# Kernel tuning notes

Hardware: AMD Instinct MI355X
Metric: run time of the kernel (lower is better)

Reference implementation:

```python
import jax, jax.numpy as jnp
import numpy as np

B, S, H = 2, 2048, 1024
E, K = 16, 2
CF = 1.5
IMP_THRESH = 0.5
CAP_MAX = int(B * S * CF * K / E)  # 768, capacity when adaptive_k == K


def setup_inputs() -> dict:
    key = jax.random.key(0)
    ks = jax.random.split(key, 8)
    def xavier(k, shape):
        fan_in, fan_out = shape[0], shape[1]
        std = np.sqrt(2.0 / (fan_in + fan_out))
        return jax.random.normal(k, shape, dtype=jnp.float32) * std
    return {
        'hidden_states': jax.random.normal(ks[0], (B, S, H), dtype=jnp.float32),
        # router: Linear(H,H) -> ReLU -> Linear(H,E)
        'W1': xavier(ks[1], (H, H)), 'b1': jnp.zeros((H,), jnp.float32),
        'W2': xavier(ks[2], (H, E)), 'b2': jnp.zeros((E,), jnp.float32),
        # importance predictor: Linear(H,H//2) -> ReLU -> Linear(H//2,1) -> Sigmoid
        'Wi1': xavier(ks[3], (H, H // 2)), 'bi1': jnp.zeros((H // 2,), jnp.float32),
        'Wi2': xavier(ks[4], (H // 2, 1)), 'bi2': jnp.zeros((1,), jnp.float32),
        # top_k predictor: Linear(H+1,H//4) -> ReLU -> Linear(H//4,K) -> Softmax
        'Wt1': xavier(ks[5], (H + 1, H // 4)), 'bt1': jnp.zeros((H // 4,), jnp.float32),
        'Wt2': xavier(ks[6], (H // 4, K)), 'bt2': jnp.zeros((K,), jnp.float32),
    }


def reference(hidden_states, W1, b1, W2, b2, Wi1, bi1, Wi2, bi2, Wt1, bt1, Wt2, bt2):
    # importance scores [B,S]
    imp_h = jax.nn.relu(hidden_states @ Wi1 + bi1)
    importance = jax.nn.sigmoid(jnp.squeeze(imp_h @ Wi2 + bi2, -1))

    # adaptive top-k (traced scalar in [1, K])
    avg_feat = hidden_states.mean((0, 1))                       # [H]
    combined = jnp.concatenate([avg_feat, importance.mean()[None]])  # [H+1]
    tk_probs = jax.nn.softmax(jax.nn.relu(combined @ Wt1 + bt1) @ Wt2 + bt2)
    adaptive_k = jnp.minimum(jnp.argmax(tk_probs) + 1, K).astype(jnp.int32)

    # router logits -> probs -> top-k
    logits = jax.nn.relu(hidden_states @ W1 + b1) @ W2 + b2     # [B,S,E]
    router_probs = jax.nn.softmax(logits, axis=-1)
    topk_p, topk_i = jax.lax.top_k(router_probs, K)             # [B,S,K], sorted desc

    # only the first adaptive_k slots are active (== torch.topk with k=adaptive_k)
    slot_valid = (jnp.arange(K) < adaptive_k)                   # [K] bool
    p = topk_p * slot_valid.astype(topk_p.dtype)
    p = p / (p.sum(-1, keepdims=True) + 1e-8)

    # capacity-limited dispatch/combine (vectorized version of the b,s,k loop)
    cap_eff = jnp.floor(jnp.float32(B * S) * CF * adaptive_k.astype(jnp.float32) / E).astype(jnp.int32)
    N = B * S * K
    e_flat = topk_i.reshape(N)                                  # expert id per (b,s,k) in loop order
    p_flat = p.reshape(N)
    valid = jnp.broadcast_to(slot_valid, (B * S, K)).reshape(N)
    oh = jax.nn.one_hot(e_flat, E, dtype=jnp.float32) * valid[:, None].astype(jnp.float32)  # [N,E]
    # position within expert = running count of earlier valid assignments to same expert
    pos = (jnp.cumsum(oh, axis=0)[jnp.arange(N), e_flat] - 1.0).astype(jnp.int32)
    write = valid & (pos >= 0) & (pos < cap_eff)
    pos_c = jnp.clip(pos, 0, CAP_MAX - 1)
    t_idx = jnp.arange(N) // K                                  # flat token index
    wf = write.astype(p_flat.dtype)
    dispatch = jnp.zeros((B * S, E, CAP_MAX), p.dtype).at[t_idx, e_flat, pos_c].add(wf)
    combine = jnp.zeros((B * S, E, CAP_MAX), p.dtype).at[t_idx, e_flat, pos_c].add(wf * p_flat)
    dispatch = dispatch.reshape(B, S, E, CAP_MAX)
    combine = combine.reshape(B, S, E, CAP_MAX)

    # load-balancing aux loss
    prob_per_expert = router_probs.mean((0, 1))                 # [E]
    usage = oh.sum(0) / (jnp.float32(B * S) * adaptive_k.astype(jnp.float32))
    aux_loss = jnp.sum(prob_per_expert * usage) * E

    # importance re-weighting of combine tensor
    iw = (importance > IMP_THRESH).astype(combine.dtype)
    combine = combine * (1.0 + iw[:, :, None, None])

    return dispatch, combine, router_probs, aux_loss, importance
```

## Files before the change

kernel.cpp:

```cpp
#include <hip/hip_runtime.h>
#include <math.h>

#define TOK   4096
#define HD    1024
#define NEXP  16
#define CAPM  768

static const size_t DISP_OFF = 0;
static const size_t COMB_OFF = 50331648;
static const size_t RP_OFF   = 100663296;
static const size_t AUX_OFF  = 100728832;
static const size_t IMP_OFF  = 100728833;

#define WS_IMPZ   0
#define WS_COLSUM 4096
#define WS_T1PRE  5120
#define WS_PROBS  5376
#define WS_AK     5392
#define WS_TOPKP  5400
#define WS_TOPKI  13592
#define WS_ZEROF  5400

typedef float v4f __attribute__((ext_vector_type(4)));

__global__ __launch_bounds__(256) void kZero(v4f* __restrict__ p, int n4)
{
    const v4f z = (v4f)(0.f);
    const int stride = gridDim.x * 256;
    for (int i = blockIdx.x * 256 + threadIdx.x; i < n4; i += stride)
        __builtin_nontemporal_store(z, p + i);
}

#define KA_ROW(i, AX) \
    acc[i][0] = fmaf(AX, f0.x, acc[i][0]); \
    acc[i][1] = fmaf(AX, f0.y, acc[i][1]); \
    acc[i][2] = fmaf(AX, f0.z, acc[i][2]); \
    acc[i][3] = fmaf(AX, f0.w, acc[i][3]); \
    acc[i][4] = fmaf(AX, f1.x, acc[i][4]); \
    acc[i][5] = fmaf(AX, f1.y, acc[i][5]); \
    acc[i][6] = fmaf(AX, f1.z, acc[i][6]); \
    acc[i][7] = fmaf(AX, f1.w, acc[i][7]);

__global__ __launch_bounds__(256, 4) void kA(
    const float* __restrict__ x, const float* __restrict__ W1,
    const float* __restrict__ b1, const float* __restrict__ Wi1,
    const float* __restrict__ bi1, const float* __restrict__ Wi2,
    float* __restrict__ h1out, float* __restrict__ impz)
{
    __shared__ __align__(16) float As[2][16][68];
    __shared__ __align__(16) float Bs[2][16][128];
    __shared__ float red[64];

    const int tid = threadIdx.x;
    const int tx = tid & 15;
    const int ty = tid >> 4;
    const int n0 = blockIdx.x * 128;
    const int m0 = blockIdx.y * 64;
    const bool isW1 = (n0 < HD);
    const float* __restrict__ Bp = isW1 ? (W1 + n0) : (Wi1 + (n0 - HD));
    const int ldb = isW1 ? 1024 : 512;

    const int am  = tid >> 2;
    const int akq = tid & 3;
    const int br = tid >> 5;
    const int bq = tid & 31;

    if (tid < 64) red[tid] = 0.f;

    float acc[4][8];
#pragma unroll
    for (int i = 0; i < 4; ++i)
#pragma unroll
        for (int j = 0; j < 8; ++j) acc[i][j] = 0.f;

    const float* pA = x + (size_t)(m0 + am) * HD + akq * 4;
    const float* pB = Bp + (size_t)br * ldb + bq * 4;

    float4 ra  = *(const float4*)(pA);
    float4 rb0 = *(const float4*)(pB);
    float4 rb1 = *(const float4*)(pB + (size_t)8 * ldb);
    {
        As[0][akq * 4 + 0][am] = ra.x;
        As[0][akq * 4 + 1][am] = ra.y;
        As[0][akq * 4 + 2][am] = ra.z;
        As[0][akq * 4 + 3][am] = ra.w;
        *(float4*)&Bs[0][br][bq * 4]     = rb0;
        *(float4*)&Bs[0][br + 8][bq * 4] = rb1;
    }
    __syncthreads();

#pragma unroll 1
    for (int kt = 0; kt < 64; ++kt) {
        const int buf = kt & 1;
        if (kt < 63) {
            const int ko = (kt + 1) * 16;
            ra  = *(const float4*)(pA + ko);
            rb0 = *(const float4*)(pB + (size_t)(ko + 0) * ldb);
            rb1 = *(const float4*)(pB + (size_t)(ko + 8) * ldb);
        }
#pragma unroll 8
        for (int kk = 0; kk < 16; ++kk) {
            const float4 a  = *(const float4*)&As[buf][kk][ty * 4];
            const float4 f0 = *(const float4*)&Bs[buf][kk][tx * 4];
            const float4 f1 = *(const float4*)&Bs[buf][kk][tx * 4 + 64];
            KA_ROW(0, a.x)
            KA_ROW(1, a.y)
            KA_ROW(2, a.z)
            KA_ROW(3, a.w)
        }
        if (kt < 63) {
            const int nb = buf ^ 1;
            As[nb][akq * 4 + 0][am] = ra.x;
            As[nb][akq * 4 + 1][am] = ra.y;
            As[nb][akq * 4 + 2][am] = ra.z;
            As[nb][akq * 4 + 3][am] = ra.w;
            *(float4*)&Bs[nb][br][bq * 4]     = rb0;
            *(float4*)&Bs[nb][br + 8][bq * 4] = rb1;
            __syncthreads();
        }
    }

    if (isW1) {
        const float4 bb0 = *(const float4*)(b1 + n0 + tx * 4);
        const float4 bb1 = *(const float4*)(b1 + n0 + tx * 4 + 64);
        const float bvv[8] = { bb0.x, bb0.y, bb0.z, bb0.w, bb1.x, bb1.y, bb1.z, bb1.w };
#pragma unroll
        for (int i = 0; i < 4; ++i) {
            const int m = m0 + ty * 4 + i;
            float4 o0, o1;
            o0.x = fmaxf(acc[i][0] + bvv[0], 0.f);
            o0.y = fmaxf(acc[i][1] + bvv[1], 0.f);
            o0.z = fmaxf(acc[i][2] + bvv[2], 0.f);
            o0.w = fmaxf(acc[i][3] + bvv[3], 0.f);
            o1.x = fmaxf(acc[i][4] + bvv[4], 0.f);
            o1.y = fmaxf(acc[i][5] + bvv[5], 0.f);
            o1.z = fmaxf(acc[i][6] + bvv[6], 0.f);
            o1.w = fmaxf(acc[i][7] + bvv[7], 0.f);
            *(float4*)(h1out + (size_t)m * HD + n0 + tx * 4)      = o0;
            *(float4*)(h1out + (size_t)m * HD + n0 + tx * 4 + 64) = o1;
        }
    } else {
        const int nW = n0 - HD;
        const float4 bb0 = *(const float4*)(bi1 + nW + tx * 4);
        const float4 bb1 = *(const float4*)(bi1 + nW + tx * 4 + 64);
        const float4 w0  = *(const float4*)(Wi2 + nW + tx * 4);
        const float4 w1  = *(const float4*)(Wi2 + nW + tx * 4 + 64);
        const float bvv[8] = { bb0.x, bb0.y, bb0.z, bb0.w, bb1.x, bb1.y, bb1.z, bb1.w };
        const float wvv[8] = { w0.x, w0.y, w0.z, w0.w, w1.x, w1.y, w1.z, w1.w };
        __syncthreads();
#pragma unroll
        for (int i = 0; i < 4; ++i) {
            float s = 0.f;
#pragma unroll
            for (int j = 0; j < 8; ++j)
                s += fmaxf(acc[i][j] + bvv[j], 0.f) * wvv[j];
            atomicAdd(&red[ty * 4 + i], s);
        }
        __syncthreads();
        if (tid < 64) atomicAdd(&impz[m0 + tid], red[tid]);
    }
}

__global__ void kSig(const float* __restrict__ impz, const float* __restrict__ bi2,
                     float* __restrict__ impOut)
{
    const int t = blockIdx.x * 256 + threadIdx.x;
    const float z = impz[t] + bi2[0];
    impOut[t] = 1.f / (1.f + expf(-z));
}

__global__ void kAvg(const float* __restrict__ x, float* __restrict__ colsum)
{
    const int c = blockIdx.x * 256 + threadIdx.x;
    const int r0 = blockIdx.y * 64;
    float s = 0.f;
    for (int r = r0; r < r0 + 64; ++r) s += x[(size_t)r * HD + c];
    atomicAdd(&colsum[c], s);
}

__global__ void kTk1(const float* __restrict__ colsum, const float* __restrict__ Wt1,
                     float* __restrict__ t1pre)
{
    const int j = threadIdx.x;
    const int i0 = blockIdx.x * 32;
    float s = 0.f;
    for (int i = i0; i < i0 + 32; ++i)
        s = fmaf(colsum[i] * (1.f / TOK), Wt1[i * 256 + j], s);
    atomicAdd(&t1pre[j], s);
}

__global__ void kTk2(const float* __restrict__ imp, const float* __restrict__ t1pre,
                     const float* __restrict__ Wt1, const float* __restrict__ bt1,
                     const float* __restrict__ Wt2, const float* __restrict__ bt2,
                     int* __restrict__ akOut)
{
    __shared__ float sm[256];
    const int tid = threadIdx.x;
    float s = 0.f;
    for (int i = 0; i < 16; ++i) s += imp[tid + i * 256];
    sm[tid] = s;
    __syncthreads();
    for (int off = 128; off > 0; off >>= 1) {
        if (tid < off) sm[tid] += sm[tid + off];
        __syncthreads();
    }
    const float imp_mean = sm[0] * (1.f / TOK);
    __syncthreads();
    const float t1 = fmaxf(t1pre[tid] + imp_mean * Wt1[1024 * 256 + tid] + bt1[tid], 0.f);
    sm[tid] = t1 * Wt2[tid * 2 + 0];
    __syncthreads();
    for (int off = 128; off > 0; off >>= 1) {
        if (tid < off) sm[tid] += sm[tid + off];
        __syncthreads();
    }
    const float l0 = sm[0] + bt2[0];
    __syncthreads();
    sm[tid] = t1 * Wt2[tid * 2 + 1];
    __syncthreads();
    for (int off = 128; off > 0; off >>= 1) {
        if (tid < off) sm[tid] += sm[tid + off];
        __syncthreads();
    }
    const float l1 = sm[0] + bt2[1];
    if (tid == 0) akOut[0] = (l1 > l0) ? 2 : 1;
}

__global__ __launch_bounds__(256) void kLog(
    const float* __restrict__ h1, const float* __restrict__ W2,
    const float* __restrict__ b2, float* __restrict__ rp,
    float* __restrict__ topkP, int* __restrict__ topkI,
    float* __restrict__ probsum)
{
    __shared__ float lg[16][17];
    __shared__ float ex[16][17];
    __shared__ float ps[16];
    const int tid = threadIdx.x;
    const int e  = tid & 15;
    const int tt = tid >> 4;
    const int t  = blockIdx.x * 16 + tt;
    const float* __restrict__ hrow = h1 + (size_t)t * HD;
    float s0 = 0.f, s1 = 0.f, s2 = 0.f, s3 = 0.f;
#pragma unroll 4
    for (int k = 0; k < HD; k += 4) {
        const float4 h = *(const float4*)(hrow + k);
        s0 = fmaf(h.x, W2[(k + 0) * NEXP + e], s0);
        s1 = fmaf(h.y, W2[(k + 1) * NEXP + e], s1);
        s2 = fmaf(h.z, W2[(k + 2) * NEXP + e], s2);
        s3 = fmaf(h.w, W2[(k + 3) * NEXP + e], s3);
    }
    const float logit = (s0 + s1) + (s2 + s3) + b2[e];
    lg[tt][e] = logit;
    if (tid < 16) ps[tid] = 0.f;
    __syncthreads();
    float mx = -1e30f;
#pragma unroll
    for (int j = 0; j < 16; ++j) mx = fmaxf(mx, lg[tt][j]);
    const float my_ex = expf(logit - mx);
    ex[tt][e] = my_ex;
    __syncthreads();
    float sum = 0.f;
#pragma unroll
    for (int j = 0; j < 16; ++j) sum += ex[tt][j];
    const float p = my_ex / sum;
    rp[(size_t)t * NEXP + e] = p;
    lg[tt][e] = p;
    atomicAdd(&ps[e], p);
    __syncthreads();
    if (e == 0) {
        float pv[16];
#pragma unroll
        for (int j = 0; j < 16; ++j) pv[j] = lg[tt][j];
        int i0 = 0; float v0 = pv[0];
#pragma unroll
        for (int j = 1; j < 16; ++j) if (pv[j] > v0) { v0 = pv[j]; i0 = j; }
        int i1 = -1; float v1 = -1e30f;
#pragma unroll
        for (int j = 0; j < 16; ++j) if (j != i0 && pv[j] > v1) { v1 = pv[j]; i1 = j; }
        topkP[t * 2] = v0; topkP[t * 2 + 1] = v1;
        topkI[t * 2] = i0; topkI[t * 2 + 1] = i1;
    }
    if (tid < 16) atomicAdd(&probsum[tid], ps[tid]);
}

__global__ __launch_bounds__(256) void kScan(
    const float* __restrict__ topkP, const int* __restrict__ topkI,
    const int* __restrict__ akPtr, const float* __restrict__ probsum,
    const float* __restrict__ imp, float* __restrict__ disp,
    float* __restrict__ comb, float* __restrict__ aux)
{
    __shared__ int cnt[256][16];
    __shared__ int totals[16];
    const int tid = threadIdx.x;
    const int ak = akPtr[0];
    const int cap = 384 * ak;
    int c[16];
#pragma unroll
    for (int e = 0; e < 16; ++e) c[e] = 0;
    const int n0 = tid * 32;
    for (int j = 0; j < 32; ++j) {
        const int n = n0 + j;
        if ((n & 1) < ak) c[topkI[n]]++;
    }
#pragma unroll
    for (int e = 0; e < 16; ++e) cnt[tid][e] = c[e];
    __syncthreads();
    if (tid < 16) {
        int run = 0;
        for (int i = 0; i < 256; ++i) { const int v = cnt[i][tid]; cnt[i][tid] = run; run += v; }
        totals[tid] = run;
    }
    __syncthreads();
#pragma unroll
    for (int e = 0; e < 16; ++e) c[e] = cnt[tid][e];
    for (int j = 0; j < 32; ++j) {
        const int n = n0 + j;
        const int k = n & 1;
        if (k < ak) {
            const int e = topkI[n];
            const int pos = c[e]++;
            if (pos < cap) {
                const int t = n >> 1;
                const float p0 = topkP[t * 2], p1 = topkP[t * 2 + 1];
                const float ssum = (ak == 2) ? (p0 + p1) : p0;
                const float pv = ((k == 0) ? p0 : p1) / (ssum + 1e-8f);
                const float iw = (imp[t] > 0.5f) ? 2.f : 1.f;
                const size_t idx = (size_t)t * (NEXP * CAPM) + (size_t)e * CAPM + pos;
                disp[idx] = 1.f;
                comb[idx] = pv * iw;
            }
        }
    }
    if (tid == 0) {
        float a = 0.f;
        const float invAk = 1.f / (float)(TOK * ak);
        for (int e = 0; e < 16; ++e)
            a += (probsum[e] * (1.f / TOK)) * ((float)totals[e] * invAk);
        aux[0] = a * (float)NEXP;
    }
}

extern "C" void kernel_launch(void* const* d_in, const int* in_sizes, int n_in,
                              void* d_out, int out_size, void* d_ws, size_t ws_size,
                              hipStream_t stream)
{
    const float* x   = (const float*)d_in[0];
    const float* W1  = (const float*)d_in[1];
    const float* b1  = (const float*)d_in[2];
    const float* W2  = (const float*)d_in[3];
    const float* b2  = (const float*)d_in[4];
    const float* Wi1 = (const float*)d_in[5];
    const float* bi1 = (const float*)d_in[6];
    const float* Wi2 = (const float*)d_in[7];
    const float* bi2 = (const float*)d_in[8];
    const float* Wt1 = (const float*)d_in[9];
    const float* bt1 = (const float*)d_in[10];
    const float* Wt2 = (const float*)d_in[11];
    const float* bt2 = (const float*)d_in[12];
    (void)in_sizes; (void)n_in; (void)out_size; (void)ws_size;

    float* out = (float*)d_out;
    float* wsF = (float*)d_ws;
    int*   akP = (int*)(wsF + WS_AK);

    (void)hipMemsetAsync(d_ws, 0, (size_t)WS_ZEROF * 4, stream);

    float* h1scratch = out + DISP_OFF;

    kA  <<<dim3(12, 64), 256, 0, stream>>>(x, W1, b1, Wi1, bi1, Wi2,
                                           h1scratch, wsF + WS_IMPZ);
    kSig<<<16, 256, 0, stream>>>(wsF + WS_IMPZ, bi2, out + IMP_OFF);
    kAvg<<<dim3(4, 64), 256, 0, stream>>>(x, wsF + WS_COLSUM);
    kTk1<<<32, 256, 0, stream>>>(wsF + WS_COLSUM, Wt1, wsF + WS_T1PRE);
    kTk2<<<1, 256, 0, stream>>>(out + IMP_OFF, wsF + WS_T1PRE, Wt1, bt1, Wt2, bt2, akP);
    kLog<<<256, 256, 0, stream>>>(h1scratch, W2, b2, out + RP_OFF,
                                  wsF + WS_TOPKP, (int*)(wsF + WS_TOPKI), wsF + WS_PROBS);
    kZero<<<4096, 256, 0, stream>>>((v4f*)out, 25165824);
    kScan<<<1, 256, 0, stream>>>(wsF + WS_TOPKP, (int*)(wsF + WS_TOPKI), akP,
                                 wsF + WS_PROBS, out + IMP_OFF,
                                 out + DISP_OFF, out + COMB_OFF, out + AUX_OFF);
}
```

Before: 687.4 us.

## Fold output zeroing into GEMM and logits kernels, enlarge per-thread GEMM tile

Removes the standalone zero-fill kernel over the 200MB dispatch/combine output. Extra blocks in the GEMM grid now zero the output region beyond the h1 scratch, and the logits kernel zeroes the h1 scratch rows once it has consumed them. The GEMM also moves to 128-thread blocks, each thread computing an 8x8 tile instead of 4x8, for more register reuse. The risks are higher register pressure and lower occupancy in the GEMM, and zero-fill blocks competing with the compute blocks for the GPU.

```diff
diff --git a/kernel.cpp b/kernel.cpp
--- a/kernel.cpp
+++ b/kernel.cpp
@@ -11,6 +11,11 @@
 static const size_t RP_OFF   = 100663296;
 static const size_t AUX_OFF  = 100728832;
 static const size_t IMP_OFF  = 100728833;
+
+#define Z_START4  4194304
+#define Z_END4    25165824
+#define Z_NBLK    384
+#define Z_PER     54614
 
 #define WS_IMPZ   0
 #define WS_COLSUM 4096
@@ -22,14 +27,6 @@
 #define WS_ZEROF  5400
 
 typedef float v4f __attribute__((ext_vector_type(4)));
-
-__global__ __launch_bounds__(256) void kZero(v4f* __restrict__ p, int n4)
-{
-    const v4f z = (v4f)(0.f);
-    const int stride = gridDim.x * 256;
-    for (int i = blockIdx.x * 256 + threadIdx.x; i < n4; i += stride)
-        __builtin_nontemporal_store(z, p + i);
-}
 
 #define KA_ROW(i, AX) \
     acc[i][0] = fmaf(AX, f0.x, acc[i][0]); \
@@ -41,20 +38,33 @@
     acc[i][6] = fmaf(AX, f1.z, acc[i][6]); \
     acc[i][7] = fmaf(AX, f1.w, acc[i][7]);
 
-__global__ __launch_bounds__(256, 4) void kA(
+__global__ __launch_bounds__(128, 2) void kA(
     const float* __restrict__ x, const float* __restrict__ W1,
     const float* __restrict__ b1, const float* __restrict__ Wi1,
     const float* __restrict__ bi1, const float* __restrict__ Wi2,
     float* __restrict__ h1out, float* __restrict__ impz)
 {
+    const int tid = threadIdx.x;
+    const int bx = blockIdx.x;
+
+    if (bx >= 12) {
+        const int zi = (bx - 12) + 6 * blockIdx.y;
+        const int s4 = Z_START4 + zi * Z_PER;
+        int e4 = s4 + Z_PER; if (e4 > Z_END4) e4 = Z_END4;
+        v4f* p = (v4f*)h1out;
+        const v4f z = (v4f)(0.f);
+        for (int i = s4 + tid; i < e4; i += 128)
+            __builtin_nontemporal_store(z, p + i);
+        return;
+    }
+
     __shared__ __align__(16) float As[2][16][68];
     __shared__ __align__(16) float Bs[2][16][128];
     __shared__ float red[64];
 
-    const int tid = threadIdx.x;
     const int tx = tid & 15;
     const int ty = tid >> 4;
-    const int n0 = blockIdx.x * 128;
+    const int n0 = bx * 128;
     const int m0 = blockIdx.y * 64;
     const bool isW1 = (n0 < HD);
     const float* __restrict__ Bp = isW1 ? (W1 + n0) : (Wi1 + (n0 - HD));
@@ -62,30 +72,36 @@
 
     const int am  = tid >> 2;
     const int akq = tid & 3;
-    const int br = tid >> 5;
-    const int bq = tid & 31;
+    const int bk0 = tid >> 5;
+    const int bq  = tid & 31;
 
     if (tid < 64) red[tid] = 0.f;
 
-    float acc[4][8];
-#pragma unroll
-    for (int i = 0; i < 4; ++i)
+    float acc[8][8];
+#pragma unroll
+    for (int i = 0; i < 8; ++i)
 #pragma unroll
         for (int j = 0; j < 8; ++j) acc[i][j] = 0.f;
 
-    const float* pA = x + (size_t)(m0 + am) * HD + akq * 4;
-    const float* pB = Bp + (size_t)br * ldb + bq * 4;
-
-    float4 ra  = *(const float4*)(pA);
+    const float* pA0 = x + (size_t)(m0 + am) * HD + akq * 4;
+    const float* pA1 = pA0 + (size_t)32 * HD;
+    const float* pB  = Bp + (size_t)bk0 * ldb + bq * 4;
+
+    float4 ra0 = *(const float4*)(pA0);
+    float4 ra1 = *(const float4*)(pA1);
     float4 rb0 = *(const float4*)(pB);
-    float4 rb1 = *(const float4*)(pB + (size_t)8 * ldb);
+    float4 rb1 = *(const float4*)(pB + (size_t)4  * ldb);
+    float4 rb2 = *(const float4*)(pB + (size_t)8  * ldb);
+    float4 rb3 = *(const float4*)(pB + (size_t)12 * ldb);
     {
-        As[0][akq * 4 + 0][am] = ra.x;
-        As[0][akq * 4 + 1][am] = ra.y;
-        As[0][akq * 4 + 2][am] = ra.z;
-        As[0][akq * 4 + 3][am] = ra.w;
-        *(float4*)&Bs[0][br][bq * 4]     = rb0;
-        *(float4*)&Bs[0][br + 8][bq * 4] = rb1;
+        As[0][akq * 4 + 0][am] = ra0.x; As[0][akq * 4 + 1][am] = ra0.y;
+        As[0][akq * 4 + 2][am] = ra0.z; As[0][akq * 4 + 3][am] = ra0.w;
+        As[0][akq * 4 + 0][am + 32] = ra1.x; As[0][akq * 4 + 1][am + 32] = ra1.y;
+        As[0][akq * 4 + 2][am + 32] = ra1.z; As[0][akq * 4 + 3][am + 32] = ra1.w;
+        *(float4*)&Bs[0][bk0][bq * 4]      = rb0;
+        *(float4*)&Bs[0][bk0 + 4][bq * 4]  = rb1;
+        *(float4*)&Bs[0][bk0 + 8][bq * 4]  = rb2;
+        *(float4*)&Bs[0][bk0 + 12][bq * 4] = rb3;
     }
     __syncthreads();
 
@@ -94,28 +110,38 @@
         const int buf = kt & 1;
         if (kt < 63) {
             const int ko = (kt + 1) * 16;
-            ra  = *(const float4*)(pA + ko);
-            rb0 = *(const float4*)(pB + (size_t)(ko + 0) * ldb);
-            rb1 = *(const float4*)(pB + (size_t)(ko + 8) * ldb);
+            ra0 = *(const float4*)(pA0 + ko);
+            ra1 = *(const float4*)(pA1 + ko);
+            rb0 = *(const float4*)(pB + (size_t)(ko + 0)  * ldb);
+            rb1 = *(const float4*)(pB + (size_t)(ko + 4)  * ldb);
+            rb2 = *(const float4*)(pB + (size_t)(ko + 8)  * ldb);
+            rb3 = *(const float4*)(pB + (size_t)(ko + 12) * ldb);
         }
 #pragma unroll 8
         for (int kk = 0; kk < 16; ++kk) {
-            const float4 a  = *(const float4*)&As[buf][kk][ty * 4];
+            const float4 a0 = *(const float4*)&As[buf][kk][ty * 8];
+            const float4 a1 = *(const float4*)&As[buf][kk][ty * 8 + 4];
             const float4 f0 = *(const float4*)&Bs[buf][kk][tx * 4];
             const float4 f1 = *(const float4*)&Bs[buf][kk][tx * 4 + 64];
-            KA_ROW(0, a.x)
-            KA_ROW(1, a.y)
-            KA_ROW(2, a.z)
-            KA_ROW(3, a.w)
+            KA_ROW(0, a0.x)
+            KA_ROW(1, a0.y)
+            KA_ROW(2, a0.z)
+            KA_ROW(3, a0.w)
+            KA_ROW(4, a1.x)
+            KA_ROW(5, a1.y)
+            KA_ROW(6, a1.z)
+            KA_ROW(7, a1.w)
         }
         if (kt < 63) {
             const int nb = buf ^ 1;
-            As[nb][akq * 4 + 0][am] = ra.x;
-            As[nb][akq * 4 + 1][am] = ra.y;
-            As[nb][akq * 4 + 2][am] = ra.z;
-            As[nb][akq * 4 + 3][am] = ra.w;
-            *(float4*)&Bs[nb][br][bq * 4]     = rb0;
-            *(float4*)&Bs[nb][br + 8][bq * 4] = rb1;
+            As[nb][akq * 4 + 0][am] = ra0.x; As[nb][akq * 4 + 1][am] = ra0.y;
+            As[nb][akq * 4 + 2][am] = ra0.z; As[nb][akq * 4 + 3][am] = ra0.w;
+            As[nb][akq * 4 + 0][am + 32] = ra1.x; As[nb][akq * 4 + 1][am + 32] = ra1.y;
+            As[nb][akq * 4 + 2][am + 32] = ra1.z; As[nb][akq * 4 + 3][am + 32] = ra1.w;
+            *(float4*)&Bs[nb][bk0][bq * 4]      = rb0;
+            *(float4*)&Bs[nb][bk0 + 4][bq * 4]  = rb1;
+            *(float4*)&Bs[nb][bk0 + 8][bq * 4]  = rb2;
+            *(float4*)&Bs[nb][bk0 + 12][bq * 4] = rb3;
             __syncthreads();
         }
     }
@@ -125,8 +151,8 @@
         const float4 bb1 = *(const float4*)(b1 + n0 + tx * 4 + 64);
         const float bvv[8] = { bb0.x, bb0.y, bb0.z, bb0.w, bb1.x, bb1.y, bb1.z, bb1.w };
 #pragma unroll
-        for (int i = 0; i < 4; ++i) {
-            const int m = m0 + ty * 4 + i;
+        for (int i = 0; i < 8; ++i) {
+            const int m = m0 + ty * 8 + i;
             float4 o0, o1;
             o0.x = fmaxf(acc[i][0] + bvv[0], 0.f);
             o0.y = fmaxf(acc[i][1] + bvv[1], 0.f);
@@ -149,12 +175,12 @@
         const float wvv[8] = { w0.x, w0.y, w0.z, w0.w, w1.x, w1.y, w1.z, w1.w };
         __syncthreads();
 #pragma unroll
-        for (int i = 0; i < 4; ++i) {
+        for (int i = 0; i < 8; ++i) {
             float s = 0.f;
 #pragma unroll
             for (int j = 0; j < 8; ++j)
                 s += fmaxf(acc[i][j] + bvv[j], 0.f) * wvv[j];
-            atomicAdd(&red[ty * 4 + i], s);
+            atomicAdd(&red[ty * 8 + i], s);
         }
         __syncthreads();
         if (tid < 64) atomicAdd(&impz[m0 + tid], red[tid]);
@@ -226,7 +252,7 @@
 }
 
 __global__ __launch_bounds__(256) void kLog(
-    const float* __restrict__ h1, const float* __restrict__ W2,
+    float* __restrict__ h1, const float* __restrict__ W2,
     const float* __restrict__ b2, float* __restrict__ rp,
     float* __restrict__ topkP, int* __restrict__ topkI,
     float* __restrict__ probsum)
@@ -280,6 +306,14 @@
         topkI[t * 2] = i0; topkI[t * 2 + 1] = i1;
     }
     if (tid < 16) atomicAdd(&probsum[tid], ps[tid]);
+    __syncthreads();
+    {
+        v4f* p4 = (v4f*)h1 + (size_t)blockIdx.x * 4096;
+        const v4f z = (v4f)(0.f);
+#pragma unroll
+        for (int i = 0; i < 16; ++i)
+            __builtin_nontemporal_store(z, p4 + tid + i * 256);
+    }
 }
 
 __global__ __launch_bounds__(256) void kScan(
@@ -366,7 +400,7 @@
 
     float* h1scratch = out + DISP_OFF;
 
-    kA  <<<dim3(12, 64), 256, 0, stream>>>(x, W1, b1, Wi1, bi1, Wi2,
+    kA  <<<dim3(18, 64), 128, 0, stream>>>(x, W1, b1, Wi1, bi1, Wi2,
                                            h1scratch, wsF + WS_IMPZ);
     kSig<<<16, 256, 0, stream>>>(wsF + WS_IMPZ, bi2, out + IMP_OFF);
     kAvg<<<dim3(4, 64), 256, 0, stream>>>(x, wsF + WS_COLSUM);
@@ -374,7 +408,6 @@
     kTk2<<<1, 256, 0, stream>>>(out + IMP_OFF, wsF + WS_T1PRE, Wt1, bt1, Wt2, bt2, akP);
     kLog<<<256, 256, 0, stream>>>(h1scratch, W2, b2, out + RP_OFF,
                                   wsF + WS_TOPKP, (int*)(wsF + WS_TOPKI), wsF + WS_PROBS);
-    kZero<<<4096, 256, 0, stream>>>((v4f*)out, 25165824);
     kScan<<<1, 256, 0, stream>>>(wsF + WS_TOPKP, (int*)(wsF + WS_TOPKI), akP,
                                  wsF + WS_PROBS, out + IMP_OFF,
                                  out + DISP_OFF, out + COMB_OFF, out + AUX_OFF);
```

New measurement: 697.0 us. About the same (+1.4%).
